# Performance work log

Hardware: AMD Instinct MI355X
Metric: run time of the kernel (lower is better)

## Reference

```python
import jax, jax.numpy as jnp
import numpy as np

B, N, F_IN = 32, 1024, 128
H1, H2, OUT = 64, 32, 10
EDGE_P = 0.01  # edge probability for random adjacency


def setup_inputs() -> dict:
    key = jax.random.key(0)
    ks = jax.random.split(key, 16)
    x = jax.random.normal(ks[0], (B, N, F_IN), dtype=jnp.float32)
    # dense binary adjacency per graph (module consumes dense [N,N] adj)
    adj = (jax.random.uniform(ks[1], (B, N, N)) < EDGE_P).astype(jnp.float32)
    mask = jnp.ones((B, N, 1), dtype=jnp.float32)
    s = 0.05
    W1a = jax.random.normal(ks[2], (F_IN, H1), dtype=jnp.float32) * s
    b1a = jnp.zeros((H1,), dtype=jnp.float32)
    W2a = jax.random.normal(ks[3], (H1, H1), dtype=jnp.float32) * s
    b2a = jnp.zeros((H1,), dtype=jnp.float32)
    W1b = jax.random.normal(ks[4], (H1, H2), dtype=jnp.float32) * s
    b1b = jnp.zeros((H2,), dtype=jnp.float32)
    W2b = jax.random.normal(ks[5], (H2, H2), dtype=jnp.float32) * s
    b2b = jnp.zeros((H2,), dtype=jnp.float32)
    Wfc = jax.random.normal(ks[6], (H2, OUT), dtype=jnp.float32) * s
    bfc = jnp.zeros((OUT,), dtype=jnp.float32)
    return dict(x=x, adj=adj, mask=mask, W1a=W1a, b1a=b1a, W2a=W2a, b2a=b2a,
                W1b=W1b, b1b=b1b, W2b=W2b, b2b=b2b, Wfc=Wfc, bfc=bfc)


def _gin_layer(h, adj, mask, Wa, ba, Wb, bb, eps=0.0):
    # neighbor sum aggregation: neigh[b,i] = sum_j adj[b,i,j] * h[b,j]
    neigh = jnp.einsum('bij,bjf->bif', adj, h)
    z = (1.0 + eps) * h + neigh
    z = jax.nn.relu(z @ Wa + ba) @ Wb + bb  # 2-layer MLP
    return z * mask  # zero out padded nodes


def reference(x, adj, mask, W1a, b1a, W2a, b2a, W1b, b1b, W2b, b2b, Wfc, bfc):
    h = _gin_layer(x, adj, mask, W1a, b1a, W2a, b2a)   # [B,N,64]
    h = _gin_layer(h, adj, mask, W1b, b1b, W2b, b2b)   # [B,N,32]
    g = jnp.max(h, axis=1)                              # graph readout [B,32]
    return g @ Wfc + bfc                                # [B,OUT] (dropout = eval identity)
```

## Files before the change

kernel.cpp:

```cpp
#include <hip/hip_runtime.h>
#include <cstdint>
#include <cstddef>


#define CAP 64

typedef float v4f __attribute__((ext_vector_type(4)));

__device__ __forceinline__ float rl(float x, int l) {
  return __int_as_float(__builtin_amdgcn_readlane(__float_as_int(x), l));
}

__global__ __launch_bounds__(256) void k_proj1(
    const float* __restrict__ x, const float* __restrict__ W1a,
    float* __restrict__ u) {
  __shared__ float sW[128 * 64];
  for (int t = threadIdx.x; t < 128 * 64; t += 256) sW[t] = W1a[t];
  __syncthreads();
  int lane = threadIdx.x & 63;
  int wid  = threadIdx.x >> 6;
  int row0 = (blockIdx.x * 4 + wid) * 8;
  row0 = __builtin_amdgcn_readfirstlane(row0);
  const float* xr = x + (size_t)row0 * 128;
  float acc[8] = {0, 0, 0, 0, 0, 0, 0, 0};
  for (int kc = 0; kc < 32; ++kc) {
    v4f xv[8];
    #pragma unroll
    for (int r = 0; r < 8; ++r)
      xv[r] = *(const v4f*)(xr + r * 128 + kc * 4);
    #pragma unroll
    for (int j = 0; j < 4; ++j) {
      float w = sW[(kc * 4 + j) * 64 + lane];
      #pragma unroll
      for (int r = 0; r < 8; ++r)
        acc[r] = fmaf(xv[r][j], w, acc[r]);
    }
  }
  #pragma unroll
  for (int r = 0; r < 8; ++r)
    u[(size_t)(row0 + r) * 64 + lane] = acc[r];
}

__global__ __launch_bounds__(256) void k_scan(
    const float* __restrict__ adj, int* __restrict__ nbr,
    int* __restrict__ deg) {
  int lane = threadIdx.x & 63;
  int node = blockIdx.x * 4 + (threadIdx.x >> 6);
  const v4f* arow = (const v4f*)(adj + (size_t)node * 1024);
  int* out = nbr + node * CAP;
  v4f a[4];
  #pragma unroll
  for (int c = 0; c < 4; ++c)
    a[c] = __builtin_nontemporal_load(arow + c * 64 + lane);
  int cnt = 0;
  #pragma unroll
  for (int c = 0; c < 4; ++c) {
    #pragma unroll
    for (int comp = 0; comp < 4; ++comp) {
      bool hit = (a[c][comp] != 0.0f);
      unsigned long long m = __ballot(hit);
      if (hit) {
        int below = __builtin_amdgcn_mbcnt_hi(
            (unsigned)(m >> 32),
            __builtin_amdgcn_mbcnt_lo((unsigned)m, 0));
        int pos = cnt + below;
        if (pos < CAP) out[pos] = ((c * 64 + lane) << 2) + comp;
      }
      cnt += __popcll(m);
    }
  }
  if (lane == 0) deg[node] = cnt < CAP ? cnt : CAP;
}

__global__ __launch_bounds__(256) void k_gathA(
    const float* __restrict__ u, const int* __restrict__ nbr,
    const int* __restrict__ deg, const float* __restrict__ mask,
    const float* __restrict__ b1a, const float* __restrict__ W2a,
    const float* __restrict__ b2a, const float* __restrict__ W1b,
    float* __restrict__ v) {
  int lane = threadIdx.x & 63;
  int f = lane & 31, hh = lane >> 5;
  float w2[64];
  #pragma unroll
  for (int k = 0; k < 64; ++k) w2[k] = W2a[k * 64 + lane];
  float w1b[32];
  #pragma unroll
  for (int k0 = 0; k0 < 32; ++k0) w1b[k0] = W1b[(hh * 32 + k0) * 32 + f];
  float ba1 = b1a[lane], ba2 = b2a[lane];
  int gw = blockIdx.x * 4 + (threadIdx.x >> 6);
  #pragma unroll 1
  for (int it = 0; it < 4; ++it) {
    int node = gw * 4 + it;
    const float* ub = u + (size_t)(node & ~1023) * 64;
    int d = deg[node];
    int nli = nbr[node * CAP + lane];
    float s[8] = {0, 0, 0, 0, 0, 0, 0, 0};
    int rounds = (d + 7) >> 3;
    for (int rr = 0; rr < rounds; ++rr) {
      int base = rr << 3;
      #pragma unroll
      for (int i = 0; i < 8; ++i) {
        int t = base + i;
        int j = __builtin_amdgcn_readlane(nli, t);
        bool ok = t < d;
        j = ok ? j : 0;
        float val = ub[j * 64 + lane];
        s[i] += ok ? val : 0.0f;
      }
    }
    float acc = ub[(node & 1023) * 64 + lane]
              + (((s[0] + s[1]) + (s[2] + s[3])) + ((s[4] + s[5]) + (s[6] + s[7])));
    float r = fmaxf(acc + ba1, 0.0f);
    float h0 = 0, h1 = 0, h2c = 0, h3c = 0;
    #pragma unroll
    for (int k = 0; k < 64; k += 4) {
      h0  = fmaf(rl(r, k    ), w2[k    ], h0);
      h1  = fmaf(rl(r, k + 1), w2[k + 1], h1);
      h2c = fmaf(rl(r, k + 2), w2[k + 2], h2c);
      h3c = fmaf(rl(r, k + 3), w2[k + 3], h3c);
    }
    float h2 = (ba2 + ((h0 + h1) + (h2c + h3c))) * mask[node];
    float vp0 = 0, vp1 = 0;
    #pragma unroll
    for (int k0 = 0; k0 < 32; k0 += 2) {
      vp0 = fmaf(__shfl(h2, hh * 32 + k0    ), w1b[k0    ], vp0);
      vp1 = fmaf(__shfl(h2, hh * 32 + k0 + 1), w1b[k0 + 1], vp1);
    }
    float vp = vp0 + vp1;
    vp += __shfl_xor(vp, 32);
    if (hh == 0) v[node * 32 + f] = vp;
  }
}

__global__ __launch_bounds__(256) void k_gathB(
    const float* __restrict__ v, const int* __restrict__ nbr,
    const int* __restrict__ deg, const float* __restrict__ mask,
    const float* __restrict__ b1b, const float* __restrict__ W2b,
    const float* __restrict__ b2b, float* __restrict__ h3) {
  int lane = threadIdx.x & 63;
  int f = lane & 31, hh = lane >> 5;
  float w2b[32];
  #pragma unroll
  for (int k = 0; k < 32; ++k) w2b[k] = W2b[k * 32 + f];
  float bb1 = b1b[f], bb2 = b2b[f];
  int gw = blockIdx.x * 4 + (threadIdx.x >> 6);
  #pragma unroll 1
  for (int it = 0; it < 4; ++it) {
    int node = gw * 4 + it;
    const float* vb = v + (size_t)(node & ~1023) * 32;
    int d = deg[node];
    int nli = nbr[node * CAP + lane];
    float s[8] = {0, 0, 0, 0, 0, 0, 0, 0};
    int rounds = (d + 15) >> 4;
    for (int rr = 0; rr < rounds; ++rr) {
      int base = rr << 4;
      #pragma unroll
      for (int i = 0; i < 8; ++i) {
        int t = base + (i << 1) + hh;
        int j = __shfl(nli, t);
        bool ok = t < d;
        j = ok ? j : 0;
        float val = vb[j * 32 + f];
        s[i] += ok ? val : 0.0f;
      }
    }
    float acc = ((s[0] + s[1]) + (s[2] + s[3])) + ((s[4] + s[5]) + (s[6] + s[7]));
    acc += __shfl_xor(acc, 32);
    float pre = vb[(node & 1023) * 32 + f] + acc + bb1;
    float r = fmaxf(pre, 0.0f);
    float o0 = 0, o1 = 0, o2 = 0, o3 = 0;
    #pragma unroll
    for (int k = 0; k < 32; k += 4) {
      o0 = fmaf(rl(r, k    ), w2b[k    ], o0);
      o1 = fmaf(rl(r, k + 1), w2b[k + 1], o1);
      o2 = fmaf(rl(r, k + 2), w2b[k + 2], o2);
      o3 = fmaf(rl(r, k + 3), w2b[k + 3], o3);
    }
    float o = (bb2 + ((o0 + o1) + (o2 + o3))) * mask[node];
    if (hh == 0) h3[node * 32 + f] = o;
  }
}

__global__ __launch_bounds__(1024) void k_readout(
    const float* __restrict__ h3, const float* __restrict__ Wfc,
    const float* __restrict__ bfc, float* __restrict__ out) {
  __shared__ float red[32][33];
  __shared__ float g[32];
  int b = blockIdx.x;
  int f = threadIdx.x & 31, c = threadIdx.x >> 5;
  const float* hb = h3 + (size_t)b * 1024 * 32;
  float m = -3.4e38f;
  for (int r0 = 0; r0 < 32; ++r0)
    m = fmaxf(m, hb[(c * 32 + r0) * 32 + f]);
  red[c][f] = m;
  __syncthreads();
  if (c == 0) {
    float mm = red[0][f];
    #pragma unroll
    for (int k = 1; k < 32; ++k) mm = fmaxf(mm, red[k][f]);
    g[f] = mm;
  }
  __syncthreads();
  if (threadIdx.x < 10) {
    float o = bfc[threadIdx.x];
    #pragma unroll
    for (int k = 0; k < 32; ++k)
      o = fmaf(g[k], Wfc[k * 10 + threadIdx.x], o);
    out[b * 10 + threadIdx.x] = o;
  }
}

extern "C" void kernel_launch(void* const* d_in, const int* in_sizes, int n_in,
                              void* d_out, int out_size, void* d_ws, size_t ws_size,
                              hipStream_t stream) {
  const float* x    = (const float*)d_in[0];
  const float* adj  = (const float*)d_in[1];
  const float* mask = (const float*)d_in[2];
  const float* W1a  = (const float*)d_in[3];
  const float* b1a  = (const float*)d_in[4];
  const float* W2a  = (const float*)d_in[5];
  const float* b2a  = (const float*)d_in[6];
  const float* W1b  = (const float*)d_in[7];
  const float* b1b  = (const float*)d_in[8];
  const float* W2b  = (const float*)d_in[9];
  const float* b2b  = (const float*)d_in[10];
  const float* Wfc  = (const float*)d_in[11];
  const float* bfc  = (const float*)d_in[12];
  float* out = (float*)d_out;

  char* ws = (char*)d_ws;
  float* u   = (float*)(ws);
  float* v   = (float*)(ws + (8u << 20));
  int*   nbr = (int*)  (ws + (12u << 20));
  int*   deg = (int*)  (ws + (20u << 20));
  float* h3  = (float*)(ws);

  hipLaunchKernelGGL(k_scan,    dim3(8192), dim3(256),  0, stream, adj, nbr, deg);
  hipLaunchKernelGGL(k_proj1,   dim3(1024), dim3(256),  0, stream, x, W1a, u);
  hipLaunchKernelGGL(k_gathA,   dim3(2048), dim3(256),  0, stream,
                     u, nbr, deg, mask, b1a, W2a, b2a, W1b, v);
  hipLaunchKernelGGL(k_gathB,   dim3(2048), dim3(256),  0, stream,
                     v, nbr, deg, mask, b1b, W2b, b2b, h3);
  hipLaunchKernelGGL(k_readout, dim3(32),   dim3(1024), 0, stream,
                     h3, Wfc, bfc, out);
}
```

Baseline: 321.7 us.

## Merge scan and projection kernels; process two nodes per wave with LDS weights

Folds the adjacency scan and the first projection into one launch, with blocks split by index, so the two independent stages can overlap and one launch is saved. The gather kernels now handle two nodes per wave at the same time instead of looping over four. This interleaves independent gathers for more memory-level parallelism, and the grids double to cover the same nodes. Weights move from per-thread register arrays to shared memory, which lowers register pressure at the cost of LDS reads. The scan half of the merged kernel also now statically reserves 32KB of shared memory, which may limit its occupancy.

```diff
diff --git a/kernel.cpp b/kernel.cpp
--- a/kernel.cpp
+++ b/kernel.cpp
@@ -11,65 +11,64 @@
   return __int_as_float(__builtin_amdgcn_readlane(__float_as_int(x), l));
 }
 
-__global__ __launch_bounds__(256) void k_proj1(
+__global__ __launch_bounds__(256) void k_scanproj(
     const float* __restrict__ x, const float* __restrict__ W1a,
-    float* __restrict__ u) {
+    float* __restrict__ u,
+    const float* __restrict__ adj, int* __restrict__ nbr,
+    int* __restrict__ deg) {
   __shared__ float sW[128 * 64];
-  for (int t = threadIdx.x; t < 128 * 64; t += 256) sW[t] = W1a[t];
-  __syncthreads();
   int lane = threadIdx.x & 63;
   int wid  = threadIdx.x >> 6;
-  int row0 = (blockIdx.x * 4 + wid) * 8;
-  row0 = __builtin_amdgcn_readfirstlane(row0);
-  const float* xr = x + (size_t)row0 * 128;
-  float acc[8] = {0, 0, 0, 0, 0, 0, 0, 0};
-  for (int kc = 0; kc < 32; ++kc) {
-    v4f xv[8];
-    #pragma unroll
-    for (int r = 0; r < 8; ++r)
-      xv[r] = *(const v4f*)(xr + r * 128 + kc * 4);
-    #pragma unroll
-    for (int j = 0; j < 4; ++j) {
-      float w = sW[(kc * 4 + j) * 64 + lane];
+  if (blockIdx.x < 1024) {
+    for (int t = threadIdx.x; t < 128 * 64; t += 256) sW[t] = W1a[t];
+    __syncthreads();
+    int row0 = (blockIdx.x * 4 + wid) * 8;
+    row0 = __builtin_amdgcn_readfirstlane(row0);
+    const float* xr = x + (size_t)row0 * 128;
+    float acc[8] = {0, 0, 0, 0, 0, 0, 0, 0};
+    for (int kc = 0; kc < 32; ++kc) {
+      v4f xv[8];
       #pragma unroll
       for (int r = 0; r < 8; ++r)
-        acc[r] = fmaf(xv[r][j], w, acc[r]);
-    }
-  }
-  #pragma unroll
-  for (int r = 0; r < 8; ++r)
-    u[(size_t)(row0 + r) * 64 + lane] = acc[r];
-}
-
-__global__ __launch_bounds__(256) void k_scan(
-    const float* __restrict__ adj, int* __restrict__ nbr,
-    int* __restrict__ deg) {
-  int lane = threadIdx.x & 63;
-  int node = blockIdx.x * 4 + (threadIdx.x >> 6);
-  const v4f* arow = (const v4f*)(adj + (size_t)node * 1024);
-  int* out = nbr + node * CAP;
-  v4f a[4];
-  #pragma unroll
-  for (int c = 0; c < 4; ++c)
-    a[c] = __builtin_nontemporal_load(arow + c * 64 + lane);
-  int cnt = 0;
-  #pragma unroll
-  for (int c = 0; c < 4; ++c) {
-    #pragma unroll
-    for (int comp = 0; comp < 4; ++comp) {
-      bool hit = (a[c][comp] != 0.0f);
-      unsigned long long m = __ballot(hit);
-      if (hit) {
-        int below = __builtin_amdgcn_mbcnt_hi(
-            (unsigned)(m >> 32),
-            __builtin_amdgcn_mbcnt_lo((unsigned)m, 0));
-        int pos = cnt + below;
-        if (pos < CAP) out[pos] = ((c * 64 + lane) << 2) + comp;
+        xv[r] = *(const v4f*)(xr + r * 128 + kc * 4);
+      #pragma unroll
+      for (int j = 0; j < 4; ++j) {
+        float w = sW[(kc * 4 + j) * 64 + lane];
+        #pragma unroll
+        for (int r = 0; r < 8; ++r)
+          acc[r] = fmaf(xv[r][j], w, acc[r]);
       }
-      cnt += __popcll(m);
-    }
-  }
-  if (lane == 0) deg[node] = cnt < CAP ? cnt : CAP;
+    }
+    #pragma unroll
+    for (int r = 0; r < 8; ++r)
+      u[(size_t)(row0 + r) * 64 + lane] = acc[r];
+  } else {
+    int node = (blockIdx.x - 1024) * 4 + wid;
+    const v4f* arow = (const v4f*)(adj + (size_t)node * 1024);
+    int* outp = nbr + node * CAP;
+    v4f a[4];
+    #pragma unroll
+    for (int c = 0; c < 4; ++c)
+      a[c] = __builtin_nontemporal_load(arow + c * 64 + lane);
+    int cnt = 0;
+    #pragma unroll
+    for (int c = 0; c < 4; ++c) {
+      #pragma unroll
+      for (int comp = 0; comp < 4; ++comp) {
+        bool hit = (a[c][comp] != 0.0f);
+        unsigned long long m = __ballot(hit);
+        if (hit) {
+          int below = __builtin_amdgcn_mbcnt_hi(
+              (unsigned)(m >> 32),
+              __builtin_amdgcn_mbcnt_lo((unsigned)m, 0));
+          int pos = cnt + below;
+          if (pos < CAP) outp[pos] = ((c * 64 + lane) << 2) + comp;
+        }
+        cnt += __popcll(m);
+      }
+    }
+    if (lane == 0) deg[node] = cnt < CAP ? cnt : CAP;
+  }
 }
 
 __global__ __launch_bounds__(256) void k_gathA(
@@ -78,57 +77,72 @@
     const float* __restrict__ b1a, const float* __restrict__ W2a,
     const float* __restrict__ b2a, const float* __restrict__ W1b,
     float* __restrict__ v) {
+  __shared__ float sW2[64 * 64];
+  __shared__ float sW1b[64 * 32];
+  for (int t = threadIdx.x; t < 64 * 64; t += 256) sW2[t] = W2a[t];
+  for (int t = threadIdx.x; t < 64 * 32; t += 256) sW1b[t] = W1b[t];
+  __syncthreads();
   int lane = threadIdx.x & 63;
   int f = lane & 31, hh = lane >> 5;
-  float w2[64];
-  #pragma unroll
-  for (int k = 0; k < 64; ++k) w2[k] = W2a[k * 64 + lane];
-  float w1b[32];
-  #pragma unroll
-  for (int k0 = 0; k0 < 32; ++k0) w1b[k0] = W1b[(hh * 32 + k0) * 32 + f];
   float ba1 = b1a[lane], ba2 = b2a[lane];
   int gw = blockIdx.x * 4 + (threadIdx.x >> 6);
-  #pragma unroll 1
-  for (int it = 0; it < 4; ++it) {
-    int node = gw * 4 + it;
-    const float* ub = u + (size_t)(node & ~1023) * 64;
-    int d = deg[node];
-    int nli = nbr[node * CAP + lane];
-    float s[8] = {0, 0, 0, 0, 0, 0, 0, 0};
-    int rounds = (d + 7) >> 3;
-    for (int rr = 0; rr < rounds; ++rr) {
-      int base = rr << 3;
-      #pragma unroll
-      for (int i = 0; i < 8; ++i) {
-        int t = base + i;
-        int j = __builtin_amdgcn_readlane(nli, t);
-        bool ok = t < d;
-        j = ok ? j : 0;
-        float val = ub[j * 64 + lane];
-        s[i] += ok ? val : 0.0f;
-      }
-    }
-    float acc = ub[(node & 1023) * 64 + lane]
-              + (((s[0] + s[1]) + (s[2] + s[3])) + ((s[4] + s[5]) + (s[6] + s[7])));
-    float r = fmaxf(acc + ba1, 0.0f);
-    float h0 = 0, h1 = 0, h2c = 0, h3c = 0;
-    #pragma unroll
-    for (int k = 0; k < 64; k += 4) {
-      h0  = fmaf(rl(r, k    ), w2[k    ], h0);
-      h1  = fmaf(rl(r, k + 1), w2[k + 1], h1);
-      h2c = fmaf(rl(r, k + 2), w2[k + 2], h2c);
-      h3c = fmaf(rl(r, k + 3), w2[k + 3], h3c);
-    }
-    float h2 = (ba2 + ((h0 + h1) + (h2c + h3c))) * mask[node];
-    float vp0 = 0, vp1 = 0;
-    #pragma unroll
-    for (int k0 = 0; k0 < 32; k0 += 2) {
-      vp0 = fmaf(__shfl(h2, hh * 32 + k0    ), w1b[k0    ], vp0);
-      vp1 = fmaf(__shfl(h2, hh * 32 + k0 + 1), w1b[k0 + 1], vp1);
-    }
-    float vp = vp0 + vp1;
-    vp += __shfl_xor(vp, 32);
-    if (hh == 0) v[node * 32 + f] = vp;
+  int n0 = gw * 2, n1 = n0 + 1;
+  const float* ub = u + (size_t)(n0 & ~1023) * 64;
+  int d0 = deg[n0], d1 = deg[n1];
+  int nl0 = nbr[n0 * CAP + lane], nl1 = nbr[n1 * CAP + lane];
+  float s0[8] = {0,0,0,0,0,0,0,0}, s1[8] = {0,0,0,0,0,0,0,0};
+  int dmax = d0 > d1 ? d0 : d1;
+  int rounds = (dmax + 7) >> 3;
+  for (int rr = 0; rr < rounds; ++rr) {
+    int base = rr << 3;
+    #pragma unroll
+    for (int i = 0; i < 8; ++i) {
+      int t = base + i;
+      int j0 = __builtin_amdgcn_readlane(nl0, t);
+      int j1 = __builtin_amdgcn_readlane(nl1, t);
+      bool ok0 = t < d0, ok1 = t < d1;
+      j0 = ok0 ? j0 : 0;  j1 = ok1 ? j1 : 0;
+      float v0 = ub[j0 * 64 + lane];
+      float v1 = ub[j1 * 64 + lane];
+      s0[i] += ok0 ? v0 : 0.0f;
+      s1[i] += ok1 ? v1 : 0.0f;
+    }
+  }
+  float acc0 = ub[(n0 & 1023) * 64 + lane]
+             + (((s0[0]+s0[1])+(s0[2]+s0[3]))+((s0[4]+s0[5])+(s0[6]+s0[7])));
+  float acc1 = ub[(n1 & 1023) * 64 + lane]
+             + (((s1[0]+s1[1])+(s1[2]+s1[3]))+((s1[4]+s1[5])+(s1[6]+s1[7])));
+  float r0 = fmaxf(acc0 + ba1, 0.0f);
+  float r1 = fmaxf(acc1 + ba1, 0.0f);
+  float a0=0,a1=0,a2=0,a3=0, c0=0,c1=0,c2=0,c3=0;
+  #pragma unroll
+  for (int k = 0; k < 64; k += 4) {
+    float w0 = sW2[(k    ) * 64 + lane];
+    float w1 = sW2[(k + 1) * 64 + lane];
+    float w2 = sW2[(k + 2) * 64 + lane];
+    float w3 = sW2[(k + 3) * 64 + lane];
+    a0 = fmaf(rl(r0, k    ), w0, a0);  c0 = fmaf(rl(r1, k    ), w0, c0);
+    a1 = fmaf(rl(r0, k + 1), w1, a1);  c1 = fmaf(rl(r1, k + 1), w1, c1);
+    a2 = fmaf(rl(r0, k + 2), w2, a2);  c2 = fmaf(rl(r1, k + 2), w2, c2);
+    a3 = fmaf(rl(r0, k + 3), w3, a3);  c3 = fmaf(rl(r1, k + 3), w3, c3);
+  }
+  float h20 = (ba2 + ((a0 + a1) + (a2 + a3))) * mask[n0];
+  float h21 = (ba2 + ((c0 + c1) + (c2 + c3))) * mask[n1];
+  float p00=0,p01=0, p10=0,p11=0;
+  #pragma unroll
+  for (int k0 = 0; k0 < 32; k0 += 2) {
+    float w0 = sW1b[(hh * 32 + k0    ) * 32 + f];
+    float w1 = sW1b[(hh * 32 + k0 + 1) * 32 + f];
+    p00 = fmaf(__shfl(h20, hh * 32 + k0    ), w0, p00);
+    p01 = fmaf(__shfl(h20, hh * 32 + k0 + 1), w1, p01);
+    p10 = fmaf(__shfl(h21, hh * 32 + k0    ), w0, p10);
+    p11 = fmaf(__shfl(h21, hh * 32 + k0 + 1), w1, p11);
+  }
+  float vp0 = p00 + p01;  vp0 += __shfl_xor(vp0, 32);
+  float vp1 = p10 + p11;  vp1 += __shfl_xor(vp1, 32);
+  if (hh == 0) {
+    v[n0 * 32 + f] = vp0;
+    v[n1 * 32 + f] = vp1;
   }
 }
 
@@ -137,47 +151,58 @@
     const int* __restrict__ deg, const float* __restrict__ mask,
     const float* __restrict__ b1b, const float* __restrict__ W2b,
     const float* __restrict__ b2b, float* __restrict__ h3) {
+  __shared__ float sW2b[32 * 32];
+  for (int t = threadIdx.x; t < 32 * 32; t += 256) sW2b[t] = W2b[t];
+  __syncthreads();
   int lane = threadIdx.x & 63;
   int f = lane & 31, hh = lane >> 5;
-  float w2b[32];
-  #pragma unroll
-  for (int k = 0; k < 32; ++k) w2b[k] = W2b[k * 32 + f];
   float bb1 = b1b[f], bb2 = b2b[f];
   int gw = blockIdx.x * 4 + (threadIdx.x >> 6);
-  #pragma unroll 1
-  for (int it = 0; it < 4; ++it) {
-    int node = gw * 4 + it;
-    const float* vb = v + (size_t)(node & ~1023) * 32;
-    int d = deg[node];
-    int nli = nbr[node * CAP + lane];
-    float s[8] = {0, 0, 0, 0, 0, 0, 0, 0};
-    int rounds = (d + 15) >> 4;
-    for (int rr = 0; rr < rounds; ++rr) {
-      int base = rr << 4;
-      #pragma unroll
-      for (int i = 0; i < 8; ++i) {
-        int t = base + (i << 1) + hh;
-        int j = __shfl(nli, t);
-        bool ok = t < d;
-        j = ok ? j : 0;
-        float val = vb[j * 32 + f];
-        s[i] += ok ? val : 0.0f;
-      }
-    }
-    float acc = ((s[0] + s[1]) + (s[2] + s[3])) + ((s[4] + s[5]) + (s[6] + s[7]));
-    acc += __shfl_xor(acc, 32);
-    float pre = vb[(node & 1023) * 32 + f] + acc + bb1;
-    float r = fmaxf(pre, 0.0f);
-    float o0 = 0, o1 = 0, o2 = 0, o3 = 0;
-    #pragma unroll
-    for (int k = 0; k < 32; k += 4) {
-      o0 = fmaf(rl(r, k    ), w2b[k    ], o0);
-      o1 = fmaf(rl(r, k + 1), w2b[k + 1], o1);
-      o2 = fmaf(rl(r, k + 2), w2b[k + 2], o2);
-      o3 = fmaf(rl(r, k + 3), w2b[k + 3], o3);
-    }
-    float o = (bb2 + ((o0 + o1) + (o2 + o3))) * mask[node];
-    if (hh == 0) h3[node * 32 + f] = o;
+  int n0 = gw * 2, n1 = n0 + 1;
+  const float* vb = v + (size_t)(n0 & ~1023) * 32;
+  int d0 = deg[n0], d1 = deg[n1];
+  int nl0 = nbr[n0 * CAP + lane], nl1 = nbr[n1 * CAP + lane];
+  float s0[8] = {0,0,0,0,0,0,0,0}, s1[8] = {0,0,0,0,0,0,0,0};
+  int dmax = d0 > d1 ? d0 : d1;
+  int rounds = (dmax + 15) >> 4;
+  for (int rr = 0; rr < rounds; ++rr) {
+    int base = rr << 4;
+    #pragma unroll
+    for (int i = 0; i < 8; ++i) {
+      int t = base + (i << 1) + hh;
+      int j0 = __shfl(nl0, t);
+      int j1 = __shfl(nl1, t);
+      bool ok0 = t < d0, ok1 = t < d1;
+      j0 = ok0 ? j0 : 0;  j1 = ok1 ? j1 : 0;
+      float v0 = vb[j0 * 32 + f];
+      float v1 = vb[j1 * 32 + f];
+      s0[i] += ok0 ? v0 : 0.0f;
+      s1[i] += ok1 ? v1 : 0.0f;
+    }
+  }
+  float acc0 = ((s0[0]+s0[1])+(s0[2]+s0[3]))+((s0[4]+s0[5])+(s0[6]+s0[7]));
+  float acc1 = ((s1[0]+s1[1])+(s1[2]+s1[3]))+((s1[4]+s1[5])+(s1[6]+s1[7]));
+  acc0 += __shfl_xor(acc0, 32);
+  acc1 += __shfl_xor(acc1, 32);
+  float r0 = fmaxf(vb[(n0 & 1023) * 32 + f] + acc0 + bb1, 0.0f);
+  float r1 = fmaxf(vb[(n1 & 1023) * 32 + f] + acc1 + bb1, 0.0f);
+  float a0=0,a1=0,a2=0,a3=0, c0=0,c1=0,c2=0,c3=0;
+  #pragma unroll
+  for (int k = 0; k < 32; k += 4) {
+    float w0 = sW2b[(k    ) * 32 + f];
+    float w1 = sW2b[(k + 1) * 32 + f];
+    float w2 = sW2b[(k + 2) * 32 + f];
+    float w3 = sW2b[(k + 3) * 32 + f];
+    a0 = fmaf(rl(r0, k    ), w0, a0);  c0 = fmaf(rl(r1, k    ), w0, c0);
+    a1 = fmaf(rl(r0, k + 1), w1, a1);  c1 = fmaf(rl(r1, k + 1), w1, c1);
+    a2 = fmaf(rl(r0, k + 2), w2, a2);  c2 = fmaf(rl(r1, k + 2), w2, c2);
+    a3 = fmaf(rl(r0, k + 3), w3, a3);  c3 = fmaf(rl(r1, k + 3), w3, c3);
+  }
+  float o0 = (bb2 + ((a0 + a1) + (a2 + a3))) * mask[n0];
+  float o1 = (bb2 + ((c0 + c1) + (c2 + c3))) * mask[n1];
+  if (hh == 0) {
+    h3[n0 * 32 + f] = o0;
+    h3[n1 * 32 + f] = o1;
   }
 }
 
@@ -235,12 +260,12 @@
   int*   deg = (int*)  (ws + (20u << 20));
   float* h3  = (float*)(ws);
 
-  hipLaunchKernelGGL(k_scan,    dim3(8192), dim3(256),  0, stream, adj, nbr, deg);
-  hipLaunchKernelGGL(k_proj1,   dim3(1024), dim3(256),  0, stream, x, W1a, u);
-  hipLaunchKernelGGL(k_gathA,   dim3(2048), dim3(256),  0, stream,
+  hipLaunchKernelGGL(k_scanproj, dim3(9216), dim3(256),  0, stream,
+                     x, W1a, u, adj, nbr, deg);
+  hipLaunchKernelGGL(k_gathA,    dim3(4096), dim3(256),  0, stream,
                      u, nbr, deg, mask, b1a, W2a, b2a, W1b, v);
-  hipLaunchKernelGGL(k_gathB,   dim3(2048), dim3(256),  0, stream,
+  hipLaunchKernelGGL(k_gathB,    dim3(4096), dim3(256),  0, stream,
                      v, nbr, deg, mask, b1b, W2b, b2b, h3);
-  hipLaunchKernelGGL(k_readout, dim3(32),   dim3(1024), 0, stream,
+  hipLaunchKernelGGL(k_readout,  dim3(32),   dim3(1024), 0, stream,
                      h3, Wfc, bfc, out);
 }
```

New measurement: 297.8 us. -7.4%, faster.
